# Kernel tuning notes

Measured on AMD Instinct MI355X. Metric: run time of the kernel, lower is better.

Reference implementation:

```python
import jax, jax.numpy as jnp
import numpy as np

DIM = 1024
INTER = 1024
E = 8            # n_routed_experts
TOP_K = 2        # n_activated_experts
ROUTE_SCALE = 1.0
B, S = 2, 1024


def setup_inputs() -> dict:
    key = jax.random.key(0)
    ks = jax.random.split(key, 8)
    scale = 0.02
    x = jax.random.normal(ks[0], (B, S, DIM), dtype=jnp.float32)
    gate_w = jax.random.normal(ks[1], (DIM, E), dtype=jnp.float32) * scale
    w1 = jax.random.normal(ks[2], (E, DIM, INTER), dtype=jnp.float32) * scale
    w2 = jax.random.normal(ks[3], (E, INTER, DIM), dtype=jnp.float32) * scale
    w3 = jax.random.normal(ks[4], (E, DIM, INTER), dtype=jnp.float32) * scale
    sw1 = jax.random.normal(ks[5], (DIM, INTER), dtype=jnp.float32) * scale
    sw2 = jax.random.normal(ks[6], (INTER, DIM), dtype=jnp.float32) * scale
    sw3 = jax.random.normal(ks[7], (DIM, INTER), dtype=jnp.float32) * scale
    return {"x": x, "gate_w": gate_w, "w1": w1, "w2": w2, "w3": w3,
            "sw1": sw1, "sw2": sw2, "sw3": sw3}


def reference(x, gate_w, w1, w2, w3, sw1, sw2, sw3):
    b, s, d = x.shape
    xt = x.reshape(-1, d)                      # [T, D]
    T = xt.shape[0]

    # --- TokenChoiceTopKRouter (score_func='softmax') ---
    scores = jax.nn.softmax((xt @ gate_w).astype(jnp.float32), axis=-1)  # [T, E]
    top_scores, top_idx = jax.lax.top_k(scores, TOP_K)                   # [T, K]
    top_scores = top_scores * ROUTE_SCALE

    # Dense combine weights [T, E]: scatter top-k routing weights per token.
    cw = jnp.zeros((T, E), dtype=xt.dtype)
    cw = cw.at[jnp.arange(T)[:, None], top_idx].set(top_scores.astype(xt.dtype))

    # --- GroupedExperts: SwiGLU per routed expert ---
    h1 = jnp.einsum('td,edh->teh', xt, w1)     # [T, E, INTER]
    h3 = jnp.einsum('td,edh->teh', xt, w3)
    h = jax.nn.silu(h1) * h3
    expert_out = jnp.einsum('teh,ehd->ted', h, w2)   # [T, E, D]

    # Combine: weighted sum over activated experts (zero weight elsewhere).
    routed = jnp.einsum('ted,te->td', expert_out, cw)

    # --- Shared expert (runs on all tokens) ---
    shared = (jax.nn.silu(xt @ sw1) * (xt @ sw3)) @ sw2

    return (routed + shared).reshape(b, s, d)
```

## Files before the change

kernel.cpp:

```cpp
#include <hip/hip_runtime.h>
#include <hip/hip_bf16.h>
#include <cstdint>
#include <cstddef>

#define DIM   1024
#define INTER 1024
#define NT    2048

typedef __attribute__((ext_vector_type(4))) float  f32x4;
typedef __attribute__((ext_vector_type(8))) short  s16x8;
typedef __attribute__((ext_vector_type(8))) unsigned short u16x8;

#define WS_CNT    0u
#define WS_SLOT   256u
#define WS_ASSIGN 33024u
#define WS_WT     65792u
#define WS_WTS2   98560u
#define WS_XB     131584u
#define WS_H      4325888u
#define WS_W1T    16908800u
#define WS_W3T    33686016u
#define WS_W2T    50463232u
#define WS_SW1T   67240448u
#define WS_SW3T   69337600u
#define WS_SW2T   71434752u
#define WS_NEED   73531904u
#define WS_OBUF   WS_W1T

__device__ __forceinline__ unsigned short f2bf(float f) {
    unsigned int u = __float_as_uint(f);
    return (unsigned short)((u + 0x7fffu + ((u >> 16) & 1u)) >> 16);
}
__device__ __forceinline__ float bf2f(unsigned short v) {
    return __uint_as_float(((unsigned int)v) << 16);
}

__device__ __forceinline__ void cp16(const void* g, void* l) {
    __builtin_amdgcn_global_load_lds((const __attribute__((address_space(1))) void*)g,
                                     (__attribute__((address_space(3))) void*)l, 16, 0, 0);
}

__device__ __forceinline__ void conv_tile(const float* __restrict__ src,
                                          unsigned short* __restrict__ dst,
                                          int r0, int c0, char* smem)
{
    float (*tile)[64][65] = (float (*)[64][65])smem;
    int tid = threadIdx.x;
    int lr = tid >> 2, lcg = (tid & 3) * 16;
    #pragma unroll
    for (int h = 0; h < 2; ++h) {
        const f32x4* srow = (const f32x4*)(src + (size_t)(r0 + lr) * 1024 + c0 + h * 64 + lcg);
        #pragma unroll
        for (int q = 0; q < 4; ++q) {
            f32x4 v = srow[q];
            #pragma unroll
            for (int j = 0; j < 4; ++j) tile[h][lr][lcg + q * 4 + j] = v[j];
        }
    }
    __syncthreads();
    int dc = tid >> 2, dkg = (tid & 3) * 16;
    #pragma unroll
    for (int h = 0; h < 2; ++h) {
        u16x8 o0, o1;
        #pragma unroll
        for (int j = 0; j < 8; ++j) o0[j] = f2bf(tile[h][dkg + j][dc]);
        #pragma unroll
        for (int j = 0; j < 8; ++j) o1[j] = f2bf(tile[h][dkg + 8 + j][dc]);
        u16x8* drow = (u16x8*)(dst + (size_t)(c0 + h * 64 + dc) * 1024 + r0 + dkg);
        drow[0] = o0; drow[1] = o1;
    }
}

__global__ __launch_bounds__(256) void kfat1(
    const float* __restrict__ x, const float* __restrict__ gw,
    const float* __restrict__ w1, const float* __restrict__ w3,
    const float* __restrict__ sw1, const float* __restrict__ sw3,
    unsigned short* __restrict__ w1t, unsigned short* __restrict__ w3t,
    unsigned short* __restrict__ sw1t, unsigned short* __restrict__ sw3t,
    int* __restrict__ assign, float2* __restrict__ wts2, unsigned short* __restrict__ xb)
{
    __shared__ __align__(16) char smem[33280];
    int bid = blockIdx.x;
    if (bid < 2304) {
        int slab = bid >> 7, t = bid & 127;
        int r0 = (t >> 3) * 64, c0 = (t & 7) * 128;
        const float* src; unsigned short* dst;
        if (slab < 8)        { src = w1 + (size_t)slab * DIM * INTER;       dst = w1t + (size_t)slab * DIM * INTER; }
        else if (slab < 16)  { src = w3 + (size_t)(slab - 8) * DIM * INTER; dst = w3t + (size_t)(slab - 8) * DIM * INTER; }
        else if (slab == 16) { src = sw1; dst = sw1t; }
        else                 { src = sw3; dst = sw3t; }
        conv_tile(src, dst, r0, c0, smem);
        return;
    }
    int wid = threadIdx.x >> 6, lane = threadIdx.x & 63;
    int t = (bid - 2304) * 4 + wid;
    const float* xrow = x + (size_t)t * DIM;

    float xr[16];
    float acc[8] = {0.f,0.f,0.f,0.f,0.f,0.f,0.f,0.f};
    #pragma unroll
    for (int j = 0; j < 16; ++j) {
        float xv = xrow[j * 64 + lane];
        xr[j] = xv;
        const f32x4* g = (const f32x4*)(gw + (size_t)(j * 64 + lane) * 8);
        f32x4 g0 = g[0], g1 = g[1];
        acc[0] += xv * g0[0]; acc[1] += xv * g0[1]; acc[2] += xv * g0[2]; acc[3] += xv * g0[3];
        acc[4] += xv * g1[0]; acc[5] += xv * g1[1]; acc[6] += xv * g1[2]; acc[7] += xv * g1[3];
    }
    #pragma unroll
    for (int j = 0; j < 16; ++j) xb[(size_t)t * DIM + j * 64 + lane] = f2bf(xr[j]);

    #pragma unroll
    for (int e = 0; e < 8; ++e) {
        float v = acc[e];
        v += __shfl_xor(v, 1);  v += __shfl_xor(v, 2);  v += __shfl_xor(v, 4);
        v += __shfl_xor(v, 8);  v += __shfl_xor(v, 16); v += __shfl_xor(v, 32);
        acc[e] = v;
    }
    float mx = acc[0];
    #pragma unroll
    for (int e = 1; e < 8; ++e) mx = fmaxf(mx, acc[e]);
    float p[8]; float se = 0.f;
    #pragma unroll
    for (int e = 0; e < 8; ++e) { p[e] = expf(acc[e] - mx); se += p[e]; }
    float inv = 1.0f / se;
    int i0 = 0; float b0 = p[0];
    #pragma unroll
    for (int e = 1; e < 8; ++e) if (p[e] > b0) { b0 = p[e]; i0 = e; }
    int i1 = -1; float b1 = -1.f;
    #pragma unroll
    for (int e = 0; e < 8; ++e) if (e != i0 && p[e] > b1) { b1 = p[e]; i1 = e; }
    if (lane == 0) {
        assign[t] = i0 | (i1 << 8);
        wts2[t] = make_float2(b0 * inv, b1 * inv);
    }
}

__global__ __launch_bounds__(256) void kscatter(const int* __restrict__ assign,
                                                const float2* __restrict__ wts2,
                                                int* __restrict__ cnt,
                                                int* __restrict__ slots,
                                                float* __restrict__ wts)
{
    __shared__ int h[8], pos[8];
    int tid = threadIdx.x, lane = tid & 63;
    if (tid < 8) h[tid] = 0;
    __syncthreads();

    for (int base = 0; base < NT; base += 256) {
        int a = assign[base + tid];
        int e0 = a & 255, e1 = (a >> 8) & 255;
        #pragma unroll
        for (int e = 0; e < 8; ++e) {
            unsigned long long m0 = __ballot(e0 == e);
            unsigned long long m1 = __ballot(e1 == e);
            if (lane == 0) {
                int c = __popcll(m0) + __popcll(m1);
                if (c) atomicAdd(&h[e], c);
            }
        }
    }
    __syncthreads();
    if (tid == 0) {
        int run = 0;
        #pragma unroll
        for (int e = 0; e < 8; ++e) {
            cnt[8 + e] = run; pos[e] = run;
            cnt[e] = h[e]; run += h[e];
        }
        cnt[16] = run;
    }
    __syncthreads();

    for (int base = 0; base < NT; base += 256) {
        int t = base + tid;
        int a = assign[t];
        float2 w = wts2[t];
        int e0 = a & 255, e1 = (a >> 8) & 255;
        unsigned long long lt = (1ull << lane) - 1ull;
        #pragma unroll
        for (int e = 0; e < 8; ++e) {
            unsigned long long m0 = __ballot(e0 == e);
            unsigned long long m1 = __ballot(e1 == e);
            int c = __popcll(m0) + __popcll(m1);
            int b = 0;
            if (lane == 0 && c) b = atomicAdd(&pos[e], c);
            b = __shfl(b, 0);
            if (e0 == e) { int r = __popcll(m0 & lt);                 slots[b + r] = t * 2;     wts[b + r] = w.x; }
            if (e1 == e) { int r = __popcll(m0) + __popcll(m1 & lt);  slots[b + r] = t * 2 + 1; wts[b + r] = w.y; }
        }
    }
}

__global__ __launch_bounds__(256) void kfat2(
    const unsigned short* __restrict__ xb,
    const unsigned short* __restrict__ w1t, const unsigned short* __restrict__ w3t,
    const unsigned short* __restrict__ sw1t, const unsigned short* __restrict__ sw3t,
    const int* __restrict__ cnt, const int* __restrict__ slots,
    unsigned short* __restrict__ hbuf,
    const float* __restrict__ w2, const float* __restrict__ sw2,
    unsigned short* __restrict__ w2t, unsigned short* __restrict__ sw2t)
{
    __shared__ __align__(16) char smem[66560];
    int z = blockIdx.z;
    if (z >= 9) {
        if (blockIdx.x >= 8) return;
        int slab = z - 9;
        const float* src; unsigned short* dst;
        if (slab < 8) { src = w2 + (size_t)slab * DIM * INTER; dst = w2t + (size_t)slab * DIM * INTER; }
        else          { src = sw2; dst = sw2t; }
        conv_tile(src, dst, blockIdx.y * 64, blockIdx.x * 128, smem);
        return;
    }

    int e = z;
    int m0 = blockIdx.y * 128;
    int n0 = blockIdx.x * 64;
    int n_rows, lbase;
    if (e < 8) { n_rows = cnt[e]; lbase = cnt[8 + e]; } else { n_rows = NT; lbase = 0; }
    if (m0 >= n_rows) return;
    int rm = min(128, n_rows - m0);

    const unsigned short* b1p = (e < 8) ? (w1t + (size_t)e * DIM * INTER) : sw1t;
    const unsigned short* b3p = (e < 8) ? (w3t + (size_t)e * DIM * INTER) : sw3t;

    char* sA  = smem;
    char* sB1 = smem + 32768;
    char* sB3 = smem + 49152;
    int* rowTok  = (int*)(smem + 65536);
    int* rowSlot = (int*)(smem + 66048);

    int tid = threadIdx.x;
    if (tid < 128) {
        int r = m0 + min(tid, rm - 1);
        int slot, tok;
        if (e < 8) { slot = slots[lbase + r]; tok = slot >> 1; }
        else       { tok = r; slot = 4096 + r; }
        rowTok[tid] = tok;
        rowSlot[tid] = slot;
    }
    __syncthreads();

    int wid = tid >> 6, lane = tid & 63;
    int wr = wid >> 1, wc = wid & 1;
    int swz_st = (((lane & 7) ^ (lane >> 3)) - (lane & 7)) * 16;

    const char* pA[4];
    #pragma unroll
    for (int q = 0; q < 4; ++q) {
        int row = (q * 4 + wid) * 8 + (lane >> 3);
        pA[q] = (const char*)(xb + (size_t)rowTok[row] * DIM) + (lane & 7) * 16 + swz_st;
    }
    const char* pB1[2]; const char* pB3[2];
    #pragma unroll
    for (int q = 0; q < 2; ++q) {
        int nrow = (q * 4 + wid) * 8 + (lane >> 3);
        pB1[q] = (const char*)(b1p + (size_t)(n0 + nrow) * DIM) + (lane & 7) * 16 + swz_st;
        pB3[q] = (const char*)(b3p + (size_t)(n0 + nrow) * DIM) + (lane & 7) * 16 + swz_st;
    }

    int loA[2], loB[2];
    #pragma unroll
    for (int ks = 0; ks < 2; ++ks) {
        int ch = ((ks * 4) + (lane >> 4)) ^ (lane & 7);
        loA[ks] = (wr * 64 + (lane & 15)) * 128 + ch * 16;
        loB[ks] = (wc * 32 + (lane & 15)) * 128 + ch * 16;
    }

    f32x4 acc1[4][2], acc3[4][2];
    #pragma unroll
    for (int m = 0; m < 4; ++m)
        #pragma unroll
        for (int n = 0; n < 2; ++n) { acc1[m][n] = (f32x4){0.f,0.f,0.f,0.f}; acc3[m][n] = (f32x4){0.f,0.f,0.f,0.f}; }

    #pragma unroll
    for (int q = 0; q < 4; ++q) { cp16(pA[q], sA + (q * 4 + wid) * 1024); pA[q] += 128; }
    #pragma unroll
    for (int q = 0; q < 2; ++q) {
        cp16(pB1[q], sB1 + (q * 4 + wid) * 1024); pB1[q] += 128;
        cp16(pB3[q], sB3 + (q * 4 + wid) * 1024); pB3[q] += 128;
    }

    for (int tt = 0; tt < 8; ++tt) {
        #pragma unroll
        for (int half = 0; half < 2; ++half) {
            if (half == 0 || tt < 7) {
                #pragma unroll
                for (int q = 0; q < 4; ++q) {
                    cp16(pA[q], sA + (half ^ 1) * 16384 + (q * 4 + wid) * 1024);
                    pA[q] += 128;
                }
                #pragma unroll
                for (int q = 0; q < 2; ++q) {
                    cp16(pB1[q], sB1 + (half ^ 1) * 8192 + (q * 4 + wid) * 1024);
                    pB1[q] += 128;
                    cp16(pB3[q], sB3 + (half ^ 1) * 8192 + (q * 4 + wid) * 1024);
                    pB3[q] += 128;
                }
                asm volatile("s_waitcnt vmcnt(8)" ::: "memory");
            } else {
                asm volatile("s_waitcnt vmcnt(0)" ::: "memory");
            }
            __builtin_amdgcn_sched_barrier(0);
            __builtin_amdgcn_s_barrier();
            __builtin_amdgcn_sched_barrier(0);

            #pragma unroll
            for (int ks = 0; ks < 2; ++ks) {
                s16x8 a[4];
                #pragma unroll
                for (int m = 0; m < 4; ++m)
                    a[m] = *(const s16x8*)(sA + half * 16384 + m * 2048 + loA[ks]);
                #pragma unroll
                for (int n = 0; n < 2; ++n) {
                    s16x8 b1 = *(const s16x8*)(sB1 + half * 8192 + n * 2048 + loB[ks]);
                    s16x8 b3 = *(const s16x8*)(sB3 + half * 8192 + n * 2048 + loB[ks]);
                    #pragma unroll
                    for (int m = 0; m < 4; ++m) {
                        acc1[m][n] = __builtin_amdgcn_mfma_f32_16x16x32_bf16(a[m], b1, acc1[m][n], 0, 0, 0);
                        acc3[m][n] = __builtin_amdgcn_mfma_f32_16x16x32_bf16(a[m], b3, acc3[m][n], 0, 0, 0);
                    }
                }
            }
            __builtin_amdgcn_sched_barrier(0);
            __builtin_amdgcn_s_barrier();
            __builtin_amdgcn_sched_barrier(0);
        }
    }

    #pragma unroll
    for (int m = 0; m < 4; ++m) {
        int rbase = wr * 64 + m * 16 + (lane >> 4) * 4;
        #pragma unroll
        for (int r = 0; r < 4; ++r) {
            int row = rbase + r;
            if (row < rm) {
                int hrow = rowSlot[row];
                #pragma unroll
                for (int n = 0; n < 2; ++n) {
                    float v1 = acc1[m][n][r], v3 = acc3[m][n][r];
                    float hv = (v1 / (1.0f + __expf(-v1))) * v3;
                    int col = n0 + wc * 32 + n * 16 + (lane & 15);
                    hbuf[(size_t)hrow * INTER + col] = f2bf(hv);
                }
            }
        }
    }
}

__global__ __launch_bounds__(256) void kgemm2(
    const unsigned short* __restrict__ hbuf,
    const unsigned short* __restrict__ w2t, const unsigned short* __restrict__ sw2t,
    const int* __restrict__ cnt, const int* __restrict__ slots,
    unsigned short* __restrict__ obuf)
{
    int e = blockIdx.z;
    int m0 = blockIdx.y * 128;
    int n0 = blockIdx.x * 64;
    int n_rows, lbase;
    if (e < 8) { n_rows = cnt[e]; lbase = cnt[8 + e]; } else { n_rows = NT; lbase = 0; }
    if (m0 >= n_rows) return;
    int rm = min(128, n_rows - m0);
    const unsigned short* bp = (e < 8) ? (w2t + (size_t)e * DIM * INTER) : sw2t;

    __shared__ __align__(16) short As[2][128 * 64];
    __shared__ __align__(16) short Bs[2][64 * 64];
    __shared__ int rowH[128];

    int tid = threadIdx.x;
    if (tid < 128) {
        int r = m0 + min(tid, rm - 1);
        rowH[tid] = (e < 8) ? slots[lbase + r] : (4096 + r);
    }
    __syncthreads();

    int wid = tid >> 6, lane = tid & 63;
    int wr = wid >> 1, wc = wid & 1;
    int swz_st = (((lane & 7) ^ (lane >> 3)) - (lane & 7)) * 16;

    const char* pA[4];
    #pragma unroll
    for (int q = 0; q < 4; ++q) {
        int row = (q * 4 + wid) * 8 + (lane >> 3);
        pA[q] = (const char*)(hbuf + (size_t)rowH[row] * INTER) + (lane & 7) * 16 + swz_st;
    }
    const char* pB[2];
    #pragma unroll
    for (int q = 0; q < 2; ++q) {
        int nrow = (q * 4 + wid) * 8 + (lane >> 3);
        pB[q] = (const char*)(bp + (size_t)(n0 + nrow) * INTER) + (lane & 7) * 16 + swz_st;
    }

    int loA[2], loB[2];
    #pragma unroll
    for (int ks = 0; ks < 2; ++ks) {
        int ch = ((ks * 4) + (lane >> 4)) ^ (lane & 7);
        loA[ks] = (wr * 64 + (lane & 15)) * 128 + ch * 16;
        loB[ks] = (wc * 32 + (lane & 15)) * 128 + ch * 16;
    }

    f32x4 acc[4][2];
    #pragma unroll
    for (int m = 0; m < 4; ++m)
        #pragma unroll
        for (int n = 0; n < 2; ++n) acc[m][n] = (f32x4){0.f,0.f,0.f,0.f};

    #pragma unroll
    for (int q = 0; q < 4; ++q) { cp16(pA[q], (char*)As + (q * 4 + wid) * 1024); pA[q] += 128; }
    #pragma unroll
    for (int q = 0; q < 2; ++q) { cp16(pB[q], (char*)Bs + (q * 4 + wid) * 1024); pB[q] += 128; }

    for (int tt = 0; tt < 8; ++tt) {
        #pragma unroll
        for (int half = 0; half < 2; ++half) {
            if (half == 0 || tt < 7) {
                #pragma unroll
                for (int q = 0; q < 4; ++q) {
                    cp16(pA[q], (char*)As + (half ^ 1) * 16384 + (q * 4 + wid) * 1024);
                    pA[q] += 128;
                }
                #pragma unroll
                for (int q = 0; q < 2; ++q) {
                    cp16(pB[q], (char*)Bs + (half ^ 1) * 8192 + (q * 4 + wid) * 1024);
                    pB[q] += 128;
                }
                asm volatile("s_waitcnt vmcnt(6)" ::: "memory");
            } else {
                asm volatile("s_waitcnt vmcnt(0)" ::: "memory");
            }
            __builtin_amdgcn_sched_barrier(0);
            __builtin_amdgcn_s_barrier();
            __builtin_amdgcn_sched_barrier(0);

            #pragma unroll
            for (int ks = 0; ks < 2; ++ks) {
                s16x8 a[4];
                #pragma unroll
                for (int m = 0; m < 4; ++m)
                    a[m] = *(const s16x8*)((const char*)As + half * 16384 + m * 2048 + loA[ks]);
                #pragma unroll
                for (int n = 0; n < 2; ++n) {
                    s16x8 b = *(const s16x8*)((const char*)Bs + half * 8192 + n * 2048 + loB[ks]);
                    #pragma unroll
                    for (int m = 0; m < 4; ++m)
                        acc[m][n] = __builtin_amdgcn_mfma_f32_16x16x32_bf16(a[m], b, acc[m][n], 0, 0, 0);
                }
            }
            __builtin_amdgcn_sched_barrier(0);
            __builtin_amdgcn_s_barrier();
            __builtin_amdgcn_sched_barrier(0);
        }
    }

    #pragma unroll
    for (int m = 0; m < 4; ++m) {
        int rbase = wr * 64 + m * 16 + (lane >> 4) * 4;
        #pragma unroll
        for (int r = 0; r < 4; ++r) {
            int row = rbase + r;
            if (row < rm) {
                int orow = rowH[row];
                #pragma unroll
                for (int n = 0; n < 2; ++n) {
                    int col = n0 + wc * 32 + n * 16 + (lane & 15);
                    obuf[(size_t)orow * DIM + col] = f2bf(acc[m][n][r]);
                }
            }
        }
    }
}

__global__ __launch_bounds__(256) void kcombine(const unsigned short* __restrict__ obuf,
                                                const float2* __restrict__ wts2,
                                                float* __restrict__ out)
{
    int gid = blockIdx.x * 256 + threadIdx.x;
    int t = gid >> 7;
    int d0 = (gid & 127) * 8;
    float2 w = wts2[t];
    u16x8 r0 = *(const u16x8*)&obuf[(size_t)(2 * t)     * DIM + d0];
    u16x8 r1 = *(const u16x8*)&obuf[(size_t)(2 * t + 1) * DIM + d0];
    u16x8 rs = *(const u16x8*)&obuf[(size_t)(4096 + t)  * DIM + d0];
    f32x4 o0, o1;
    #pragma unroll
    for (int j = 0; j < 4; ++j) o0[j] = w.x * bf2f(r0[j]) + w.y * bf2f(r1[j]) + bf2f(rs[j]);
    #pragma unroll
    for (int j = 0; j < 4; ++j) o1[j] = w.x * bf2f(r0[4+j]) + w.y * bf2f(r1[4+j]) + bf2f(rs[4+j]);
    f32x4* dst = (f32x4*)&out[(size_t)t * DIM + d0];
    dst[0] = o0; dst[1] = o1;
}

extern "C" void kernel_launch(void* const* d_in, const int* in_sizes, int n_in,
                              void* d_out, int out_size, void* d_ws, size_t ws_size,
                              hipStream_t stream) {
    const float* x      = (const float*)d_in[0];
    const float* gate_w = (const float*)d_in[1];
    const float* w1     = (const float*)d_in[2];
    const float* w2     = (const float*)d_in[3];
    const float* w3     = (const float*)d_in[4];
    const float* sw1    = (const float*)d_in[5];
    const float* sw2    = (const float*)d_in[6];
    const float* sw3    = (const float*)d_in[7];
    float* out = (float*)d_out;

    if (ws_size < (size_t)WS_NEED) return;

    char* ws = (char*)d_ws;
    int*            cnt      = (int*)(ws + WS_CNT);
    int*            slots    = (int*)(ws + WS_SLOT);
    int*            assign   = (int*)(ws + WS_ASSIGN);
    float*          wts      = (float*)(ws + WS_WT);
    float2*         wts2     = (float2*)(ws + WS_WTS2);
    unsigned short* xb       = (unsigned short*)(ws + WS_XB);
    unsigned short* hbuf     = (unsigned short*)(ws + WS_H);
    unsigned short* w1t      = (unsigned short*)(ws + WS_W1T);
    unsigned short* w3t      = (unsigned short*)(ws + WS_W3T);
    unsigned short* w2t      = (unsigned short*)(ws + WS_W2T);
    unsigned short* sw1t     = (unsigned short*)(ws + WS_SW1T);
    unsigned short* sw3t     = (unsigned short*)(ws + WS_SW3T);
    unsigned short* sw2t     = (unsigned short*)(ws + WS_SW2T);
    unsigned short* obuf     = (unsigned short*)(ws + WS_OBUF);

    kfat1<<<dim3(2816), 256, 0, stream>>>(x, gate_w, w1, w3, sw1, sw3,
                                          w1t, w3t, sw1t, sw3t, assign, wts2, xb);
    kscatter<<<dim3(1), 256, 0, stream>>>(assign, wts2, cnt, slots, wts);
    kfat2<<<dim3(16, 16, 18), 256, 0, stream>>>(xb, w1t, w3t, sw1t, sw3t, cnt, slots, hbuf,
                                                w2, sw2, w2t, sw2t);
    kgemm2<<<dim3(16, 16, 9), 256, 0, stream>>>(hbuf, w2t, sw2t, cnt, slots, obuf);
    kcombine<<<dim3(1024), 256, 0, stream>>>(obuf, wts2, out);
}
```

Before: 128.9 us.

## Replace double-buffered LDS pipeline with single-buffer load-compute loop in both GEMMs

Removes the ping-pong shared-memory double buffering and explicit vmcnt waits from both expert GEMM kernels. Each k-step now computes, syncs, issues the next tile's async copies and syncs again. This halves LDS use per block, which may allow more resident blocks. In exchange, global-load latency is no longer overlapped with MFMA work inside a block. It also relies on __syncthreads covering completion of the async cp16 copies.

```diff
diff --git a/kernel.cpp b/kernel.cpp
--- a/kernel.cpp
+++ b/kernel.cpp
@@ -201,7 +201,7 @@
     const float* __restrict__ w2, const float* __restrict__ sw2,
     unsigned short* __restrict__ w2t, unsigned short* __restrict__ sw2t)
 {
-    __shared__ __align__(16) char smem[66560];
+    __shared__ __align__(16) char smem[33792];
     int z = blockIdx.z;
     if (z >= 9) {
         if (blockIdx.x >= 8) return;
@@ -225,10 +225,10 @@
     const unsigned short* b3p = (e < 8) ? (w3t + (size_t)e * DIM * INTER) : sw3t;
 
     char* sA  = smem;
-    char* sB1 = smem + 32768;
-    char* sB3 = smem + 49152;
-    int* rowTok  = (int*)(smem + 65536);
-    int* rowSlot = (int*)(smem + 66048);
+    char* sB1 = smem + 16384;
+    char* sB3 = smem + 24576;
+    int* rowTok  = (int*)(smem + 32768);
+    int* rowSlot = (int*)(smem + 33280);
 
     int tid = threadIdx.x;
     if (tid < 128) {
@@ -280,51 +280,36 @@
         cp16(pB1[q], sB1 + (q * 4 + wid) * 1024); pB1[q] += 128;
         cp16(pB3[q], sB3 + (q * 4 + wid) * 1024); pB3[q] += 128;
     }
-
-    for (int tt = 0; tt < 8; ++tt) {
-        #pragma unroll
-        for (int half = 0; half < 2; ++half) {
-            if (half == 0 || tt < 7) {
+    __syncthreads();
+
+    for (int t = 0; t < 16; ++t) {
+        #pragma unroll
+        for (int ks = 0; ks < 2; ++ks) {
+            s16x8 a[4];
+            #pragma unroll
+            for (int m = 0; m < 4; ++m)
+                a[m] = *(const s16x8*)(sA + m * 2048 + loA[ks]);
+            #pragma unroll
+            for (int n = 0; n < 2; ++n) {
+                s16x8 b1 = *(const s16x8*)(sB1 + n * 2048 + loB[ks]);
+                s16x8 b3 = *(const s16x8*)(sB3 + n * 2048 + loB[ks]);
                 #pragma unroll
-                for (int q = 0; q < 4; ++q) {
-                    cp16(pA[q], sA + (half ^ 1) * 16384 + (q * 4 + wid) * 1024);
-                    pA[q] += 128;
-                }
-                #pragma unroll
-                for (int q = 0; q < 2; ++q) {
-                    cp16(pB1[q], sB1 + (half ^ 1) * 8192 + (q * 4 + wid) * 1024);
-                    pB1[q] += 128;
-                    cp16(pB3[q], sB3 + (half ^ 1) * 8192 + (q * 4 + wid) * 1024);
-                    pB3[q] += 128;
-                }
-                asm volatile("s_waitcnt vmcnt(8)" ::: "memory");
-            } else {
-                asm volatile("s_waitcnt vmcnt(0)" ::: "memory");
-            }
-            __builtin_amdgcn_sched_barrier(0);
-            __builtin_amdgcn_s_barrier();
-            __builtin_amdgcn_sched_barrier(0);
-
-            #pragma unroll
-            for (int ks = 0; ks < 2; ++ks) {
-                s16x8 a[4];
-                #pragma unroll
-                for (int m = 0; m < 4; ++m)
-                    a[m] = *(const s16x8*)(sA + half * 16384 + m * 2048 + loA[ks]);
-                #pragma unroll
-                for (int n = 0; n < 2; ++n) {
-                    s16x8 b1 = *(const s16x8*)(sB1 + half * 8192 + n * 2048 + loB[ks]);
-                    s16x8 b3 = *(const s16x8*)(sB3 + half * 8192 + n * 2048 + loB[ks]);
-                    #pragma unroll
-                    for (int m = 0; m < 4; ++m) {
-                        acc1[m][n] = __builtin_amdgcn_mfma_f32_16x16x32_bf16(a[m], b1, acc1[m][n], 0, 0, 0);
-                        acc3[m][n] = __builtin_amdgcn_mfma_f32_16x16x32_bf16(a[m], b3, acc3[m][n], 0, 0, 0);
-                    }
+                for (int m = 0; m < 4; ++m) {
+                    acc1[m][n] = __builtin_amdgcn_mfma_f32_16x16x32_bf16(a[m], b1, acc1[m][n], 0, 0, 0);
+                    acc3[m][n] = __builtin_amdgcn_mfma_f32_16x16x32_bf16(a[m], b3, acc3[m][n], 0, 0, 0);
                 }
             }
-            __builtin_amdgcn_sched_barrier(0);
-            __builtin_amdgcn_s_barrier();
-            __builtin_amdgcn_sched_barrier(0);
+        }
+        __syncthreads();
+        if (t < 15) {
+            #pragma unroll
+            for (int q = 0; q < 4; ++q) { cp16(pA[q], sA + (q * 4 + wid) * 1024); pA[q] += 128; }
+            #pragma unroll
+            for (int q = 0; q < 2; ++q) {
+                cp16(pB1[q], sB1 + (q * 4 + wid) * 1024); pB1[q] += 128;
+                cp16(pB3[q], sB3 + (q * 4 + wid) * 1024); pB3[q] += 128;
+            }
+            __syncthreads();
         }
     }
 
@@ -363,8 +348,8 @@
     int rm = min(128, n_rows - m0);
     const unsigned short* bp = (e < 8) ? (w2t + (size_t)e * DIM * INTER) : sw2t;
 
-    __shared__ __align__(16) short As[2][128 * 64];
-    __shared__ __align__(16) short Bs[2][64 * 64];
+    __shared__ __align__(16) short As[128 * 64];
+    __shared__ __align__(16) short Bs[64 * 64];
     __shared__ int rowH[128];
 
     int tid = threadIdx.x;
@@ -409,46 +394,30 @@
     for (int q = 0; q < 4; ++q) { cp16(pA[q], (char*)As + (q * 4 + wid) * 1024); pA[q] += 128; }
     #pragma unroll
     for (int q = 0; q < 2; ++q) { cp16(pB[q], (char*)Bs + (q * 4 + wid) * 1024); pB[q] += 128; }
-
-    for (int tt = 0; tt < 8; ++tt) {
-        #pragma unroll
-        for (int half = 0; half < 2; ++half) {
-            if (half == 0 || tt < 7) {
-                #pragma unroll
-                for (int q = 0; q < 4; ++q) {
-                    cp16(pA[q], (char*)As + (half ^ 1) * 16384 + (q * 4 + wid) * 1024);
-                    pA[q] += 128;
-                }
-                #pragma unroll
-                for (int q = 0; q < 2; ++q) {
-                    cp16(pB[q], (char*)Bs + (half ^ 1) * 8192 + (q * 4 + wid) * 1024);
-                    pB[q] += 128;
-                }
-                asm volatile("s_waitcnt vmcnt(6)" ::: "memory");
-            } else {
-                asm volatile("s_waitcnt vmcnt(0)" ::: "memory");
-            }
-            __builtin_amdgcn_sched_barrier(0);
-            __builtin_amdgcn_s_barrier();
-            __builtin_amdgcn_sched_barrier(0);
-
-            #pragma unroll
-            for (int ks = 0; ks < 2; ++ks) {
-                s16x8 a[4];
+    __syncthreads();
+
+    for (int t = 0; t < 16; ++t) {
+        #pragma unroll
+        for (int ks = 0; ks < 2; ++ks) {
+            s16x8 a[4];
+            #pragma unroll
+            for (int m = 0; m < 4; ++m)
+                a[m] = *(const s16x8*)((const char*)As + m * 2048 + loA[ks]);
+            #pragma unroll
+            for (int n = 0; n < 2; ++n) {
+                s16x8 b = *(const s16x8*)((const char*)Bs + n * 2048 + loB[ks]);
                 #pragma unroll
                 for (int m = 0; m < 4; ++m)
-                    a[m] = *(const s16x8*)((const char*)As + half * 16384 + m * 2048 + loA[ks]);
-                #pragma unroll
-                for (int n = 0; n < 2; ++n) {
-                    s16x8 b = *(const s16x8*)((const char*)Bs + half * 8192 + n * 2048 + loB[ks]);
-                    #pragma unroll
-                    for (int m = 0; m < 4; ++m)
-                        acc[m][n] = __builtin_amdgcn_mfma_f32_16x16x32_bf16(a[m], b, acc[m][n], 0, 0, 0);
-                }
+                    acc[m][n] = __builtin_amdgcn_mfma_f32_16x16x32_bf16(a[m], b, acc[m][n], 0, 0, 0);
             }
-            __builtin_amdgcn_sched_barrier(0);
-            __builtin_amdgcn_s_barrier();
-            __builtin_amdgcn_sched_barrier(0);
+        }
+        __syncthreads();
+        if (t < 15) {
+            #pragma unroll
+            for (int q = 0; q < 4; ++q) { cp16(pA[q], (char*)As + (q * 4 + wid) * 1024); pA[q] += 128; }
+            #pragma unroll
+            for (int q = 0; q < 2; ++q) { cp16(pB[q], (char*)Bs + (q * 4 + wid) * 1024); pB[q] += 128; }
+            __syncthreads();
         }
     }
 
```

After: 129.9 us. Within noise of the previous version (+0.8%).

## Pre-tile transposed weights into MFMA fragment order and load B directly to registers

Applied to the files above, without the earlier changes.

The weight conversion kernel now writes the bf16 transposed weights in a 16x32 fragment-tiled layout that matches the MFMA operand layout, with a padded LDS staging tile. The two GEMM kernels then load B operands straight from global memory into registers, double-buffered per half-step, instead of staging them through LDS. This cuts LDS traffic and LDS footprint (66 KB down to 34 KB for the first GEMM), which could allow more blocks per CU, at the cost of more vector registers and more in-flight global loads per wave.

```diff
diff --git a/kernel.cpp b/kernel.cpp
--- a/kernel.cpp
+++ b/kernel.cpp
@@ -44,30 +44,34 @@
                                           unsigned short* __restrict__ dst,
                                           int r0, int c0, char* smem)
 {
-    float (*tile)[64][65] = (float (*)[64][65])smem;
+    float* ldsf = (float*)smem;
     int tid = threadIdx.x;
-    int lr = tid >> 2, lcg = (tid & 3) * 16;
-    #pragma unroll
-    for (int h = 0; h < 2; ++h) {
-        const f32x4* srow = (const f32x4*)(src + (size_t)(r0 + lr) * 1024 + c0 + h * 64 + lcg);
-        #pragma unroll
-        for (int q = 0; q < 4; ++q) {
-            f32x4 v = srow[q];
+    {
+        int row  = tid >> 5;
+        int colw = (tid & 31) * 4;
+        const float* s = src + (size_t)(r0 + row) * 1024 + c0 + colw;
+        float* d = ldsf + row * 133 + colw;
+        #pragma unroll
+        for (int i = 0; i < 8; ++i) {
+            f32x4 v = *(const f32x4*)(s + (size_t)i * 8 * 1024);
+            *(f32x4*)(d + i * 8 * 133) = v;
+        }
+    }
+    __syncthreads();
+    {
+        int w = tid >> 6, l = tid & 63;
+        int cl = l & 15, kg = l >> 4;
+        #pragma unroll
+        for (int i = 0; i < 4; ++i) {
+            int f = w * 4 + i;
+            int ntl = f >> 1, ktl = f & 1;
+            u16x8 o;
             #pragma unroll
-            for (int j = 0; j < 4; ++j) tile[h][lr][lcg + q * 4 + j] = v[j];
-        }
-    }
-    __syncthreads();
-    int dc = tid >> 2, dkg = (tid & 3) * 16;
-    #pragma unroll
-    for (int h = 0; h < 2; ++h) {
-        u16x8 o0, o1;
-        #pragma unroll
-        for (int j = 0; j < 8; ++j) o0[j] = f2bf(tile[h][dkg + j][dc]);
-        #pragma unroll
-        for (int j = 0; j < 8; ++j) o1[j] = f2bf(tile[h][dkg + 8 + j][dc]);
-        u16x8* drow = (u16x8*)(dst + (size_t)(c0 + h * 64 + dc) * 1024 + r0 + dkg);
-        drow[0] = o0; drow[1] = o1;
+            for (int j = 0; j < 8; ++j)
+                o[j] = f2bf(ldsf[(ktl * 32 + kg * 8 + j) * 133 + ntl * 16 + cl]);
+            size_t off = ((size_t)((c0 >> 4) + ntl) * 32 + (r0 >> 5) + ktl) * 512 + l * 8;
+            *(u16x8*)(dst + off) = o;
+        }
     }
 }
 
@@ -79,7 +83,7 @@
     unsigned short* __restrict__ sw1t, unsigned short* __restrict__ sw3t,
     int* __restrict__ assign, float2* __restrict__ wts2, unsigned short* __restrict__ xb)
 {
-    __shared__ __align__(16) char smem[33280];
+    __shared__ __align__(16) char smem[34048];
     int bid = blockIdx.x;
     if (bid < 2304) {
         int slab = bid >> 7, t = bid & 127;
@@ -201,7 +205,7 @@
     const float* __restrict__ w2, const float* __restrict__ sw2,
     unsigned short* __restrict__ w2t, unsigned short* __restrict__ sw2t)
 {
-    __shared__ __align__(16) char smem[66560];
+    __shared__ __align__(16) char smem[34048];
     int z = blockIdx.z;
     if (z >= 9) {
         if (blockIdx.x >= 8) return;
@@ -224,11 +228,9 @@
     const unsigned short* b1p = (e < 8) ? (w1t + (size_t)e * DIM * INTER) : sw1t;
     const unsigned short* b3p = (e < 8) ? (w3t + (size_t)e * DIM * INTER) : sw3t;
 
-    char* sA  = smem;
-    char* sB1 = smem + 32768;
-    char* sB3 = smem + 49152;
-    int* rowTok  = (int*)(smem + 65536);
-    int* rowSlot = (int*)(smem + 66048);
+    char* sA = smem;
+    int* rowTok  = (int*)(smem + 32768);
+    int* rowSlot = (int*)(smem + 33280);
 
     int tid = threadIdx.x;
     if (tid < 128) {
@@ -253,18 +255,17 @@
     }
     const char* pB1[2]; const char* pB3[2];
     #pragma unroll
-    for (int q = 0; q < 2; ++q) {
-        int nrow = (q * 4 + wid) * 8 + (lane >> 3);
-        pB1[q] = (const char*)(b1p + (size_t)(n0 + nrow) * DIM) + (lane & 7) * 16 + swz_st;
-        pB3[q] = (const char*)(b3p + (size_t)(n0 + nrow) * DIM) + (lane & 7) * 16 + swz_st;
-    }
-
-    int loA[2], loB[2];
+    for (int n = 0; n < 2; ++n) {
+        int nt = (n0 >> 4) + wc * 2 + n;
+        pB1[n] = (const char*)b1p + (size_t)nt * 32768 + lane * 16;
+        pB3[n] = (const char*)b3p + (size_t)nt * 32768 + lane * 16;
+    }
+
+    int loA[2];
     #pragma unroll
     for (int ks = 0; ks < 2; ++ks) {
         int ch = ((ks * 4) + (lane >> 4)) ^ (lane & 7);
         loA[ks] = (wr * 64 + (lane & 15)) * 128 + ch * 16;
-        loB[ks] = (wc * 32 + (lane & 15)) * 128 + ch * 16;
     }
 
     f32x4 acc1[4][2], acc3[4][2];
@@ -273,13 +274,17 @@
         #pragma unroll
         for (int n = 0; n < 2; ++n) { acc1[m][n] = (f32x4){0.f,0.f,0.f,0.f}; acc3[m][n] = (f32x4){0.f,0.f,0.f,0.f}; }
 
+    s16x8 br1[2][2][2], br3[2][2][2];
+
     #pragma unroll
     for (int q = 0; q < 4; ++q) { cp16(pA[q], sA + (q * 4 + wid) * 1024); pA[q] += 128; }
     #pragma unroll
-    for (int q = 0; q < 2; ++q) {
-        cp16(pB1[q], sB1 + (q * 4 + wid) * 1024); pB1[q] += 128;
-        cp16(pB3[q], sB3 + (q * 4 + wid) * 1024); pB3[q] += 128;
-    }
+    for (int n = 0; n < 2; ++n)
+        #pragma unroll
+        for (int ks = 0; ks < 2; ++ks) {
+            br1[0][n][ks] = *(const s16x8*)(pB1[n] + ks * 1024);
+            br3[0][n][ks] = *(const s16x8*)(pB3[n] + ks * 1024);
+        }
 
     for (int tt = 0; tt < 8; ++tt) {
         #pragma unroll
@@ -291,13 +296,13 @@
                     pA[q] += 128;
                 }
                 #pragma unroll
-                for (int q = 0; q < 2; ++q) {
-                    cp16(pB1[q], sB1 + (half ^ 1) * 8192 + (q * 4 + wid) * 1024);
-                    pB1[q] += 128;
-                    cp16(pB3[q], sB3 + (half ^ 1) * 8192 + (q * 4 + wid) * 1024);
-                    pB3[q] += 128;
-                }
-                asm volatile("s_waitcnt vmcnt(8)" ::: "memory");
+                for (int n = 0; n < 2; ++n)
+                    #pragma unroll
+                    for (int ks = 0; ks < 2; ++ks) {
+                        br1[half ^ 1][n][ks] = *(const s16x8*)(pB1[n] + (half * 2 + 2 + ks) * 1024);
+                        br3[half ^ 1][n][ks] = *(const s16x8*)(pB3[n] + (half * 2 + 2 + ks) * 1024);
+                    }
+                asm volatile("s_waitcnt vmcnt(12)" ::: "memory");
             } else {
                 asm volatile("s_waitcnt vmcnt(0)" ::: "memory");
             }
@@ -313,12 +318,10 @@
                     a[m] = *(const s16x8*)(sA + half * 16384 + m * 2048 + loA[ks]);
                 #pragma unroll
                 for (int n = 0; n < 2; ++n) {
-                    s16x8 b1 = *(const s16x8*)(sB1 + half * 8192 + n * 2048 + loB[ks]);
-                    s16x8 b3 = *(const s16x8*)(sB3 + half * 8192 + n * 2048 + loB[ks]);
                     #pragma unroll
                     for (int m = 0; m < 4; ++m) {
-                        acc1[m][n] = __builtin_amdgcn_mfma_f32_16x16x32_bf16(a[m], b1, acc1[m][n], 0, 0, 0);
-                        acc3[m][n] = __builtin_amdgcn_mfma_f32_16x16x32_bf16(a[m], b3, acc3[m][n], 0, 0, 0);
+                        acc1[m][n] = __builtin_amdgcn_mfma_f32_16x16x32_bf16(a[m], br1[half][n][ks], acc1[m][n], 0, 0, 0);
+                        acc3[m][n] = __builtin_amdgcn_mfma_f32_16x16x32_bf16(a[m], br3[half][n][ks], acc3[m][n], 0, 0, 0);
                     }
                 }
             }
@@ -326,6 +329,8 @@
             __builtin_amdgcn_s_barrier();
             __builtin_amdgcn_sched_barrier(0);
         }
+        #pragma unroll
+        for (int n = 0; n < 2; ++n) { pB1[n] += 4096; pB3[n] += 4096; }
     }
 
     #pragma unroll
@@ -363,8 +368,7 @@
     int rm = min(128, n_rows - m0);
     const unsigned short* bp = (e < 8) ? (w2t + (size_t)e * DIM * INTER) : sw2t;
 
-    __shared__ __align__(16) short As[2][128 * 64];
-    __shared__ __align__(16) short Bs[2][64 * 64];
+    __shared__ __align__(16) char sA[2][16384];
     __shared__ int rowH[128];
 
     int tid = threadIdx.x;
@@ -386,17 +390,16 @@
     }
     const char* pB[2];
     #pragma unroll
-    for (int q = 0; q < 2; ++q) {
-        int nrow = (q * 4 + wid) * 8 + (lane >> 3);
-        pB[q] = (const char*)(bp + (size_t)(n0 + nrow) * INTER) + (lane & 7) * 16 + swz_st;
-    }
-
-    int loA[2], loB[2];
+    for (int n = 0; n < 2; ++n) {
+        int nt = (n0 >> 4) + wc * 2 + n;
+        pB[n] = (const char*)bp + (size_t)nt * 32768 + lane * 16;
+    }
+
+    int loA[2];
     #pragma unroll
     for (int ks = 0; ks < 2; ++ks) {
         int ch = ((ks * 4) + (lane >> 4)) ^ (lane & 7);
         loA[ks] = (wr * 64 + (lane & 15)) * 128 + ch * 16;
-        loB[ks] = (wc * 32 + (lane & 15)) * 128 + ch * 16;
     }
 
     f32x4 acc[4][2];
@@ -405,10 +408,15 @@
         #pragma unroll
         for (int n = 0; n < 2; ++n) acc[m][n] = (f32x4){0.f,0.f,0.f,0.f};
 
-    #pragma unroll
-    for (int q = 0; q < 4; ++q) { cp16(pA[q], (char*)As + (q * 4 + wid) * 1024); pA[q] += 128; }
-    #pragma unroll
-    for (int q = 0; q < 2; ++q) { cp16(pB[q], (char*)Bs + (q * 4 + wid) * 1024); pB[q] += 128; }
+    s16x8 br[2][2][2];
+
+    #pragma unroll
+    for (int q = 0; q < 4; ++q) { cp16(pA[q], (char*)sA + (q * 4 + wid) * 1024); pA[q] += 128; }
+    #pragma unroll
+    for (int n = 0; n < 2; ++n)
+        #pragma unroll
+        for (int ks = 0; ks < 2; ++ks)
+            br[0][n][ks] = *(const s16x8*)(pB[n] + ks * 1024);
 
     for (int tt = 0; tt < 8; ++tt) {
         #pragma unroll
@@ -416,15 +424,15 @@
             if (half == 0 || tt < 7) {
                 #pragma unroll
                 for (int q = 0; q < 4; ++q) {
-                    cp16(pA[q], (char*)As + (half ^ 1) * 16384 + (q * 4 + wid) * 1024);
+                    cp16(pA[q], (char*)sA + (half ^ 1) * 16384 + (q * 4 + wid) * 1024);
                     pA[q] += 128;
                 }
                 #pragma unroll
-                for (int q = 0; q < 2; ++q) {
-                    cp16(pB[q], (char*)Bs + (half ^ 1) * 8192 + (q * 4 + wid) * 1024);
-                    pB[q] += 128;
-                }
-                asm volatile("s_waitcnt vmcnt(6)" ::: "memory");
+                for (int n = 0; n < 2; ++n)
+                    #pragma unroll
+                    for (int ks = 0; ks < 2; ++ks)
+                        br[half ^ 1][n][ks] = *(const s16x8*)(pB[n] + (half * 2 + 2 + ks) * 1024);
+                asm volatile("s_waitcnt vmcnt(8)" ::: "memory");
             } else {
                 asm volatile("s_waitcnt vmcnt(0)" ::: "memory");
             }
@@ -437,19 +445,19 @@
                 s16x8 a[4];
                 #pragma unroll
                 for (int m = 0; m < 4; ++m)
-                    a[m] = *(const s16x8*)((const char*)As + half * 16384 + m * 2048 + loA[ks]);
-                #pragma unroll
-                for (int n = 0; n < 2; ++n) {
-                    s16x8 b = *(const s16x8*)((const char*)Bs + half * 8192 + n * 2048 + loB[ks]);
+                    a[m] = *(const s16x8*)((const char*)sA + half * 16384 + m * 2048 + loA[ks]);
+                #pragma unroll
+                for (int n = 0; n < 2; ++n)
                     #pragma unroll
                     for (int m = 0; m < 4; ++m)
-                        acc[m][n] = __builtin_amdgcn_mfma_f32_16x16x32_bf16(a[m], b, acc[m][n], 0, 0, 0);
-                }
+                        acc[m][n] = __builtin_amdgcn_mfma_f32_16x16x32_bf16(a[m], br[half][n][ks], acc[m][n], 0, 0, 0);
             }
             __builtin_amdgcn_sched_barrier(0);
             __builtin_amdgcn_s_barrier();
             __builtin_amdgcn_sched_barrier(0);
         }
+        #pragma unroll
+        for (int n = 0; n < 2; ++n) pB[n] += 4096;
     }
 
     #pragma unroll
```

Measured after the change: 134.6 us. 1.04x slower.
